# Performance work log

Hardware: AMD Instinct MI355X
Metric: run time of the kernel (lower is better)

## Reference

```python
import jax, jax.numpy as jnp
import numpy as np

N_SKU, N_WH, N_SUP = 100000, 5000, 2000
D_IN, D_OUT, H = 128, 64, 4
DH = D_OUT // H  # 16
E_INTRA, E_CROSS = 400000, 200000
EPS_LN = 1e-5


def setup_inputs() -> dict:
    key = jax.random.key(0)
    ks = jax.random.split(key, 40)
    f32 = jnp.float32

    def edges(k, E, n_src, n_dst):
        k1, k2 = jax.random.split(k)
        return jnp.stack([
            jax.random.randint(k1, (E,), 0, n_src),
            jax.random.randint(k2, (E,), 0, n_dst),
        ]).astype(jnp.int32)

    inp = {
        'x_sku': jax.random.normal(ks[0], (N_SKU, D_IN), f32),
        'x_wh': jax.random.normal(ks[1], (N_WH, D_IN), f32),
        'x_sup': jax.random.normal(ks[2], (N_SUP, D_IN), f32),
    }
    names = ['plant', 'pg', 'sg', 'st', 'ship', 'supply']
    for i, nm in enumerate(names):
        inp['W_' + nm] = jax.random.normal(ks[3 + 2 * i], (D_IN, D_OUT), f32) * 0.05
        inp['a_' + nm] = jax.random.normal(ks[4 + 2 * i], (2 * DH,), f32) * 0.05
    inp['proj_W'] = jax.random.normal(ks[20], (2 * D_OUT, D_OUT), f32) * 0.05
    inp['proj_b'] = jnp.zeros((D_OUT,), f32)
    inp['ln_g'] = jnp.ones((D_OUT,), f32)
    inp['ln_b'] = jnp.zeros((D_OUT,), f32)
    inp['res_W'] = jax.random.normal(ks[21], (D_IN, D_OUT), f32) * 0.05
    inp['ei_plant'] = edges(ks[22], E_INTRA, N_SKU, N_SKU)
    inp['ei_pg'] = edges(ks[23], E_INTRA, N_SKU, N_SKU)
    inp['ei_sg'] = edges(ks[24], E_INTRA, N_SKU, N_SKU)
    inp['ei_st'] = edges(ks[25], E_INTRA, N_SKU, N_SKU)
    inp['ei_ship'] = edges(ks[26], E_CROSS, N_SKU, N_WH)
    inp['ei_supply'] = edges(ks[27], E_CROSS, N_SKU, N_SUP)
    return inp


def _gat_conv(src_feat, dst_feat, ei, W, a, num_dst):
    """One-edge-type multi-head GAT: ELU edge scores, per-dst softmax, scatter-add."""
    src_i, dst_i = ei[0], ei[1]
    h_src = (src_feat @ W).reshape(-1, H, DH)  # [N_src, H, dh]
    h_dst = (dst_feat @ W).reshape(-1, H, DH)  # [N_dst, H, dh]
    hs = h_src[src_i]  # [E, H, dh] gather
    hd = h_dst[dst_i]  # [E, H, dh]
    # a^T [h_src || h_dst], shared attention vector across heads
    e = jax.nn.elu(hs @ a[:DH] + hd @ a[DH:])  # [E, H]
    # numerically stable scatter-softmax over edges grouped by dst node
    e_max = jax.lax.stop_gradient(jax.ops.segment_max(e, dst_i, num_segments=num_dst))
    e_max = jnp.where(jnp.isfinite(e_max), e_max, 0.0)
    exp_e = jnp.exp(e - e_max[dst_i])
    denom = jax.ops.segment_sum(exp_e, dst_i, num_segments=num_dst)
    alpha = exp_e / (denom[dst_i] + 1e-12)  # [E, H]
    out = jax.ops.segment_sum(alpha[..., None] * hs, dst_i, num_segments=num_dst)
    return out.reshape(num_dst, D_OUT)


def reference(x_sku, x_wh, x_sup,
              W_plant, a_plant, W_pg, a_pg, W_sg, a_sg, W_st, a_st,
              W_ship, a_ship, W_supply, a_supply,
              proj_W, proj_b, ln_g, ln_b, res_W,
              ei_plant, ei_pg, ei_sg, ei_st, ei_ship, ei_supply):
    # branch A (intra sku->sku edge types), summed into sku accumulator
    oa_sku = (_gat_conv(x_sku, x_sku, ei_plant, W_plant, a_plant, N_SKU)
              + _gat_conv(x_sku, x_sku, ei_pg, W_pg, a_pg, N_SKU)
              + _gat_conv(x_sku, x_sku, ei_sg, W_sg, a_sg, N_SKU)
              + _gat_conv(x_sku, x_sku, ei_st, W_st, a_st, N_SKU))
    ob_sku = jnp.zeros((N_SKU, D_OUT), x_sku.dtype)
    # branch B (cross edge types)
    oa_wh = jnp.zeros((N_WH, D_OUT), x_wh.dtype)
    ob_wh = _gat_conv(x_sku, x_wh, ei_ship, W_ship, a_ship, N_WH)
    oa_sup = jnp.zeros((N_SUP, D_OUT), x_sup.dtype)
    ob_sup = _gat_conv(x_sku, x_sup, ei_supply, W_supply, a_supply, N_SUP)

    def finish(x, oa, ob):
        y = jnp.concatenate([oa, ob], axis=-1) @ proj_W + proj_b + x @ res_W
        mu = y.mean(-1, keepdims=True)
        var = ((y - mu) ** 2).mean(-1, keepdims=True)
        return (y - mu) / jnp.sqrt(var + EPS_LN) * ln_g + ln_b

    return (finish(x_sku, oa_sku, ob_sku),
            finish(x_wh, oa_wh, ob_wh),
            finish(x_sup, oa_sup, ob_sup))
```

## Files before the change

### kernel.cpp

```cpp
#include <hip/hip_runtime.h>
#include <hip/hip_bf16.h>
#include <cstdint>

#define NS 100000
#define NW 5000
#define NPS 2000
#define DI 128
#define DO 64
#define NSTRIPS (NS/16)
#define NFLAT (4*NS + NW + NPS)
#define NWPAD 5008
#define NBUK 134
#define BCAP 20480
#define CHUNK 8192

#define B_CONV 6688
#define B_PACK 304
#define B_SWH  157
#define B_SSUP 63

typedef unsigned short bfu;
typedef __attribute__((ext_vector_type(8))) short s8v;
typedef __attribute__((ext_vector_type(4))) float f4v;

__device__ inline bfu f2bf(float f) {
  uint32_t u = __float_as_uint(f);
  u = (u + 0x7FFFu + ((u >> 16) & 1u)) >> 16;
  return (bfu)u;
}
__device__ inline float bf2f(bfu u) {
  return __uint_as_float((uint32_t)u << 16);
}

struct ESeg { const int* ei[6]; int E[6]; int Ecum[7]; };

__device__ inline void buk_of(int t, int d, int& b, int& loc) {
  if (t < 4)       { int f = d * 4 + t; b = f >> 12;        loc = f & 4095; }
  else if (t == 4) { b = 98 + (d >> 8);                     loc = d & 255; }
  else             { b = 118 + (d >> 7);                    loc = d & 127; }
}

struct PackA {
  const float* W[6]; const float* a[6];
  const float* resW; const float* projW;
  bfu* Bp; bfu* Rp; bfu* Pp;
};

struct K1Args {
  ESeg S; int* gCur; uint32_t* binned; int ETOT; int nbin;
  const float* x0; bfu* o0; int n0;
  const float* x1; bfu* o1; int n1;
  const float* x2; bfu* o2; int n2;
  PackA P;
  const float* xwh; const float* xsup; float* sd_wh; float* sd_sup;
};

__device__ void bin_body(const K1Args& A, int bid) {
  __shared__ int cnt[NBUK];
  __shared__ int runb[NBUK];
  const ESeg& S = A.S;
  int tid = threadIdx.x;
  int gbase = bid * CHUNK;
  if (tid < NBUK) cnt[tid] = 0;
  __syncthreads();
  #pragma unroll 4
  for (int i = 0; i < CHUNK / 256; ++i) {
    int g = gbase + i * 256 + tid;
    if (g < A.ETOT) {
      int t = 0;
      #pragma unroll
      for (int k = 0; k < 5; ++k) t += (g >= S.Ecum[k + 1]);
      int e = g - S.Ecum[t];
      int d = S.ei[t][S.E[t] + e];
      int b, loc; buk_of(t, d, b, loc);
      atomicAdd(&cnt[b], 1);
    }
  }
  __syncthreads();
  if (tid < NBUK) { runb[tid] = atomicAdd(&A.gCur[tid], cnt[tid]); cnt[tid] = 0; }
  __syncthreads();
  #pragma unroll 4
  for (int i = 0; i < CHUNK / 256; ++i) {
    int g = gbase + i * 256 + tid;
    if (g < A.ETOT) {
      int t = 0;
      #pragma unroll
      for (int k = 0; k < 5; ++k) t += (g >= S.Ecum[k + 1]);
      int e = g - S.Ecum[t];
      int sv = S.ei[t][e];
      int d  = S.ei[t][S.E[t] + e];
      int b, loc; buk_of(t, d, b, loc);
      int pos = runb[b] + atomicAdd(&cnt[b], 1);
      if (pos < BCAP)
        A.binned[(size_t)b * BCAP + pos] = ((uint32_t)loc << 17) | (uint32_t)sv;
    }
  }
}

__device__ void convert_body(const K1Args& A, int bid) {
  int t = bid * 256 + threadIdx.x;
  const float* x; bfu* o; int i;
  if (t < A.n0) { x = A.x0; o = A.o0; i = t; }
  else if (t < A.n0 + A.n1) { x = A.x1; o = A.o1; i = t - A.n0; }
  else if (t < A.n0 + A.n1 + A.n2) { x = A.x2; o = A.o2; i = t - A.n0 - A.n1; }
  else return;
  const float4* p = (const float4*)x + (size_t)i * 2;
  float4 a = p[0], b = p[1];
  uint4 v;
  v.x = (uint32_t)f2bf(a.x) | ((uint32_t)f2bf(a.y) << 16);
  v.y = (uint32_t)f2bf(a.z) | ((uint32_t)f2bf(a.w) << 16);
  v.z = (uint32_t)f2bf(b.x) | ((uint32_t)f2bf(b.y) << 16);
  v.w = (uint32_t)f2bf(b.z) | ((uint32_t)f2bf(b.w) << 16);
  ((uint4*)o)[i] = v;
}

__device__ void pack_body(const PackA& P, int bid) {
  int t = bid * 256 + threadIdx.x;
  if (t < 61440) {
    int ty = t / 10240, rem = t % 10240;
    int r = rem / 128, k = rem % 128;
    const float* W = P.W[ty]; const float* a = P.a[ty];
    float v = 0.f;
    if (r < 64) v = W[k * 64 + r];
    else if (r < 72) {
      int h = (r - 64) & 3;
      const float* av = (r < 68) ? a : (a + 16);
      #pragma unroll
      for (int m = 0; m < 16; ++m) v += W[k * 64 + h * 16 + m] * av[m];
    }
    P.Bp[ty * 10240 + rem] = f2bf(v);
  } else if (t < 69632) {
    int i = t - 61440; int j = i / 128, k = i % 128;
    P.Rp[i] = f2bf(P.resW[k * 64 + j]);
  } else if (t < 77824) {
    int i = t - 69632; int j = i / 128, k = i % 128;
    P.Pp[i] = f2bf(P.projW[k * 64 + j]);
  }
}

__device__ void scores_body(const float* __restrict__ x, const float* __restrict__ W,
                            const float* __restrict__ a, float* __restrict__ sdst,
                            int N, int bid, int nblk) {
  int tid = threadIdx.x;
  int lane = tid & 63;
  float wa[4] = {0.f, 0.f, 0.f, 0.f}, wb[4] = {0.f, 0.f, 0.f, 0.f};
  for (int m = 0; m < 16; ++m) {
    float av = a[16 + m];
    #pragma unroll
    for (int h = 0; h < 4; ++h) {
      wa[h] += W[lane * 64 + h * 16 + m] * av;
      wb[h] += W[(64 + lane) * 64 + h * 16 + m] * av;
    }
  }
  int w  = (bid * 256 + tid) >> 6;
  int nw = (nblk * 256) >> 6;
  for (int n = w; n < N; n += nw) {
    float xa = x[(size_t)n * 128 + lane], xc = x[(size_t)n * 128 + 64 + lane];
    float4 r;
    r.x = xa * wa[0] + xc * wb[0]; r.y = xa * wa[1] + xc * wb[1];
    r.z = xa * wa[2] + xc * wb[2]; r.w = xa * wa[3] + xc * wb[3];
    #pragma unroll
    for (int m = 1; m < 64; m <<= 1) {
      r.x += __shfl_xor(r.x, m); r.y += __shfl_xor(r.y, m);
      r.z += __shfl_xor(r.z, m); r.w += __shfl_xor(r.w, m);
    }
    if (lane == 0) ((float4*)sdst)[n] = r;
  }
}

__global__ __launch_bounds__(256) void k_front(K1Args A) {
  int bid = blockIdx.x;
  if (bid < A.nbin) { bin_body(A, bid); return; }
  bid -= A.nbin;
  if (bid < B_CONV) { convert_body(A, bid); return; }
  bid -= B_CONV;
  if (bid < B_PACK) { pack_body(A.P, bid); return; }
  bid -= B_PACK;
  if (bid < B_SWH) { scores_body(A.xwh, A.P.W[4], A.P.a[4], A.sd_wh, NW, bid, B_SWH); return; }
  bid -= B_SWH;
  scores_body(A.xsup, A.P.W[5], A.P.a[5], A.sd_sup, NPS, bid, B_SSUP);
}

struct MidArgs {
  const int* gCur; const uint32_t* binned; int* offs; int* ssorted;
  const bfu* xb; const bfu* Bp;
  bfu* hbAll; float* ssAll; float* sdAll; int nstrips;
};

__device__ void csr_body(const MidArgs& M, int b) {
  __shared__ int hist[4096];
  __shared__ int wq[4];
  __shared__ int wsc[4];
  __shared__ int bbase_s, cnt_s;
  int tid = threadIdx.x;
  int lane = tid & 63, wid = tid >> 6;
  int cthis = (tid < NBUK) ? min(M.gCur[tid], BCAP) : 0;
  int incx = cthis;
  #pragma unroll
  for (int d = 1; d < 64; d <<= 1) { int t = __shfl_up(incx, d); if (lane >= d) incx += t; }
  if (lane == 63) wq[wid] = incx;
  #pragma unroll
  for (int k = 0; k < 16; ++k) hist[tid * 16 + k] = 0;
  __syncthreads();
  int wp = 0;
  for (int k = 0; k < wid; ++k) wp += wq[k];
  if (tid == b) { int inclusive = incx + wp; bbase_s = inclusive - cthis; cnt_s = cthis; }
  __syncthreads();
  int cnt = cnt_s, bbase = bbase_s;
  const uint32_t* bk = M.binned + (size_t)b * BCAP;
  for (int i = tid; i < cnt; i += 256)
    atomicAdd(&hist[bk[i] >> 17], 1);
  __syncthreads();
  int t16 = tid * 16;
  int v[16], tsum = 0;
  #pragma unroll
  for (int k = 0; k < 16; ++k) { v[k] = hist[t16 + k]; tsum += v[k]; }
  int inc = tsum;
  #pragma unroll
  for (int d = 1; d < 64; d <<= 1) { int t = __shfl_up(inc, d); if (lane >= d) inc += t; }
  if (lane == 63) wsc[wid] = inc;
  __syncthreads();
  int wpre = 0;
  for (int k = 0; k < wid; ++k) wpre += wsc[k];
  int run = inc - tsum + wpre;
  #pragma unroll
  for (int k = 0; k < 16; ++k) { hist[t16 + k] = run; run += v[k]; }
  __syncthreads();
  int sbase, nslots;
  if (b < 98)        { sbase = b << 12;                nslots = min(4096, 4 * NS - sbase); }
  else if (b < 118)  { int lb = (b - 98) << 8;  sbase = 4 * NS + lb;      nslots = min(256, NW - lb); }
  else               { int lb = (b - 118) << 7; sbase = 4 * NS + NW + lb; nslots = min(128, NPS - lb); }
  for (int i = tid; i < nslots; i += 256) M.offs[sbase + i] = bbase + hist[i];
  if (b == NBUK - 1 && tid == 0) M.offs[NFLAT] = bbase + cnt;
  __syncthreads();
  for (int i = tid; i < cnt; i += 256) {
    uint32_t vv = bk[i];
    int p = atomicAdd(&hist[vv >> 17], 1);
    M.ssorted[bbase + p] = (int)(vv & 0x1FFFFu);
  }
}

__device__ void gemm_body(const MidArgs& G, int bloc) {
  int p = bloc >> 9;
  int bsub = bloc & 511;
  const bfu* Bp0 = G.Bp + (size_t)(2 * p) * 10240;
  const bfu* Bp1 = G.Bp + (size_t)(2 * p + 1) * 10240;
  bfu* hb0 = G.hbAll + (size_t)(2 * p) * NS * 64;
  bfu* hb1 = G.hbAll + (size_t)(2 * p + 1) * NS * 64;
  float* ss0 = G.ssAll + (size_t)(2 * p) * NS * 4;
  float* ss1 = G.ssAll + (size_t)(2 * p + 1) * NS * 4;
  float* sd0 = G.sdAll + (size_t)(2 * p) * NS * 4;
  float* sd1 = G.sdAll + (size_t)(2 * p + 1) * NS * 4;
  int lane = threadIdx.x & 63;
  int l15 = lane & 15, q = lane >> 4;
  int w  = (int)((bsub * 256 + threadIdx.x) >> 6);
  int nw = (512 * 256) >> 6;
  s8v bfr[10][4];
  #pragma unroll
  for (int nt = 0; nt < 5; ++nt)
    #pragma unroll
    for (int kq = 0; kq < 4; ++kq) {
      bfr[nt][kq]     = *(const s8v*)(Bp0 + (size_t)(nt * 16 + l15) * 128 + kq * 32 + q * 8);
      bfr[5 + nt][kq] = *(const s8v*)(Bp1 + (size_t)(nt * 16 + l15) * 128 + kq * 32 + q * 8);
    }
  for (int s = w; s < G.nstrips; s += nw) {
    int mb = s * 16;
    f4v acc[10];
    #pragma unroll
    for (int u = 0; u < 10; ++u) acc[u] = (f4v){0.f, 0.f, 0.f, 0.f};
    const bfu* ar = G.xb + (size_t)(mb + l15) * 128 + q * 8;
    #pragma unroll
    for (int kq = 0; kq < 4; ++kq) {
      s8v af = *(const s8v*)(ar + kq * 32);
      #pragma unroll
      for (int u = 0; u < 10; ++u)
        acc[u] = __builtin_amdgcn_mfma_f32_16x16x32_bf16(af, bfr[u][kq], acc[u], 0, 0, 0);
    }
    #pragma unroll
    for (int u = 0; u < 10; ++u) {
      int nt = (u < 5) ? u : u - 5;
      bfu* hb = (u < 5) ? hb0 : hb1;
      float* ssrc = (u < 5) ? ss0 : ss1;
      float* sdst = (u < 5) ? sd0 : sd1;
      int c = nt * 16 + l15;
      #pragma unroll
      for (int r = 0; r < 4; ++r) {
        int node = mb + q * 4 + r;
        float v = acc[u][r];
        if (c < 64)      hb[(size_t)node * 64 + c] = f2bf(v);
        else if (c < 68) ssrc[(size_t)node * 4 + (c - 64)] = v;
        else if (c < 72) sdst[(size_t)node * 4 + (c - 68)] = v;
      }
    }
  }
}

__global__ __launch_bounds__(256, 2) void k_mid(MidArgs M) {
  int bid = blockIdx.x;
  if (bid < NBUK) { csr_body(M, bid); return; }
  gemm_body(M, bid - NBUK);
}

struct AggArgs {
  const int* offs; const int* srcs;
  const bfu* hbAll;
  const float* ssAll;
  const float* sdAll;
  const float* sd_wh; const float* sd_sup;
  bfu* osku; bfu* owh; bfu* osup;
};

__global__ __launch_bounds__(256) void k_megaagg(AggArgs A) {
  int lane = threadIdx.x & 63;
  int q = lane >> 4, m = lane & 15, h = m >> 2;
  int hh = m & 3;
  int i0 = m >> 2;
  int qsh = q << 4;
  int sl0 = qsh + h;
  int w  = (int)((blockIdx.x * 256 + threadIdx.x) >> 6);
  int nw = (int)((gridDim.x * 256) >> 6);
  for (int n = w; n < NS + NW + NPS; n += nw) {
    if (n < NS) {
      const int* ob = A.offs + (size_t)n * 4;
      int4 o = *(const int4*)ob;
      int o4 = ob[4];
      int sb = (q == 0) ? o.x : (q == 1) ? o.y : (q == 2) ? o.z : o.w;
      int se = (q == 0) ? o.y : (q == 1) ? o.z : (q == 2) ? o.w : o4;
      int len = se - sb;
      int maxlen = max(max(o.y - o.x, o.z - o.y), max(o.w - o.z, o4 - o.w));
      float sdq = A.sdAll[((size_t)q * NS + n) * 4 + hh];
      uint32_t tbase = (uint32_t)q * (uint32_t)NS;
      float den = 0.f, a0 = 0.f, a1 = 0.f, a2 = 0.f, a3 = 0.f;
      for (int j0 = 0; j0 < maxlen; j0 += 16) {
        int ei = j0 + m;
        int sidx = (ei < len) ? A.srcs[sb + ei] : 0;
        int gmax = min(16, maxlen - j0);
        for (int jj = 0; jj < gmax; jj += 8) {
          int sA = __shfl(sidx, qsh + jj + i0);
          int sB = __shfl(sidx, qsh + jj + 4 + i0);
          float scA = A.ssAll[(tbase + (uint32_t)sA) * 4u + (uint32_t)hh];
          float scB = A.ssAll[(tbase + (uint32_t)sB) * 4u + (uint32_t)hh];
          float eA = scA + sdq, eB = scB + sdq;
          eA = eA > 0.f ? eA : (__expf(eA) - 1.f);
          eB = eB > 0.f ? eB : (__expf(eB) - 1.f);
          float wA = (j0 + jj + i0)     < len ? __expf(eA) : 0.f;
          float wB = (j0 + jj + 4 + i0) < len ? __expf(eB) : 0.f;
          uint2 hv[8]; float wg[8];
          #pragma unroll
          for (int i = 0; i < 8; ++i) {
            int s = __shfl(sidx, qsh + jj + i);
            uint32_t nb = tbase + (uint32_t)s;
            hv[i] = *(const uint2*)(A.hbAll + nb * 64u + (uint32_t)(m * 4));
            wg[i] = __shfl((i & 4) ? wB : wA, sl0 + ((i & 3) << 2));
          }
          #pragma unroll
          for (int i = 0; i < 8; ++i) {
            float wgt = wg[i];
            den += wgt;
            a0 = fmaf(__uint_as_float(hv[i].x << 16), wgt, a0);
            a1 = fmaf(__uint_as_float(hv[i].x & 0xffff0000u), wgt, a1);
            a2 = fmaf(__uint_as_float(hv[i].y << 16), wgt, a2);
            a3 = fmaf(__uint_as_float(hv[i].y & 0xffff0000u), wgt, a3);
          }
        }
      }
      float inv = __builtin_amdgcn_rcpf(den + 1e-12f);
      float r0 = a0 * inv, r1 = a1 * inv, r2 = a2 * inv, r3 = a3 * inv;
      r0 += __shfl_xor(r0, 16); r0 += __shfl_xor(r0, 32);
      r1 += __shfl_xor(r1, 16); r1 += __shfl_xor(r1, 32);
      r2 += __shfl_xor(r2, 16); r2 += __shfl_xor(r2, 32);
      r3 += __shfl_xor(r3, 16); r3 += __shfl_xor(r3, 32);
      if (q == 0) {
        uint2 pk;
        pk.x = (uint32_t)f2bf(r0) | ((uint32_t)f2bf(r1) << 16);
        pk.y = (uint32_t)f2bf(r2) | ((uint32_t)f2bf(r3) << 16);
        *(uint2*)(A.osku + (size_t)n * 64 + m * 4) = pk;
      }
    } else {
      int tt, nl; const float* sd; bfu* op;
      int fi;
      if (n < NS + NW) { tt = 4; nl = n - NS; fi = 4 * NS + nl; sd = A.sd_wh; op = A.owh + (size_t)nl * 64; }
      else { tt = 5; nl = n - NS - NW; fi = 4 * NS + NW + nl; sd = A.sd_sup; op = A.osup + (size_t)nl * 64; }
      int beg = A.offs[fi], end = A.offs[fi + 1];
      uint32_t tbase = (uint32_t)tt * (uint32_t)NS;
      float sdq = sd[(size_t)nl * 4 + hh];
      float den = 0.f, a0 = 0.f, a1 = 0.f, a2 = 0.f, a3 = 0.f;
      for (int cb = beg; cb < end; cb += 64) {
        int rem = min(64, end - cb);
        int sidx = (lane < rem) ? A.srcs[cb + lane] : 0;
        for (int jb = 0; jb < rem; jb += 32) {
          int eA = jb + 4 * i0 + q;
          int sA = __shfl(sidx, eA);
          int sB = __shfl(sidx, eA + 16);
          float scA = A.ssAll[(tbase + (uint32_t)sA) * 4u + (uint32_t)hh];
          float scB = A.ssAll[(tbase + (uint32_t)sB) * 4u + (uint32_t)hh];
          float fA = scA + sdq, fB = scB + sdq;
          fA = fA > 0.f ? fA : (__expf(fA) - 1.f);
          fB = fB > 0.f ? fB : (__expf(fB) - 1.f);
          float wA = (eA)      < rem ? __expf(fA) : 0.f;
          float wB = (eA + 16) < rem ? __expf(fB) : 0.f;
          uint2 hv[8]; float wg[8];
          #pragma unroll
          for (int i = 0; i < 8; ++i) {
            int s = __shfl(sidx, jb + 4 * i + q);
            uint32_t nb = tbase + (uint32_t)s;
            hv[i] = *(const uint2*)(A.hbAll + nb * 64u + (uint32_t)(m * 4));
            wg[i] = __shfl((i & 4) ? wB : wA, sl0 + ((i & 3) << 2));
          }
          #pragma unroll
          for (int i = 0; i < 8; ++i) {
            float wgt = wg[i];
            den += wgt;
            a0 = fmaf(__uint_as_float(hv[i].x << 16), wgt, a0);
            a1 = fmaf(__uint_as_float(hv[i].x & 0xffff0000u), wgt, a1);
            a2 = fmaf(__uint_as_float(hv[i].y << 16), wgt, a2);
            a3 = fmaf(__uint_as_float(hv[i].y & 0xffff0000u), wgt, a3);
          }
        }
      }
      den += __shfl_xor(den, 16); den += __shfl_xor(den, 32);
      a0 += __shfl_xor(a0, 16); a0 += __shfl_xor(a0, 32);
      a1 += __shfl_xor(a1, 16); a1 += __shfl_xor(a1, 32);
      a2 += __shfl_xor(a2, 16); a2 += __shfl_xor(a2, 32);
      a3 += __shfl_xor(a3, 16); a3 += __shfl_xor(a3, 32);
      float inv = __builtin_amdgcn_rcpf(den + 1e-12f);
      if (q == 0) {
        uint2 pk;
        pk.x = (uint32_t)f2bf(a0 * inv) | ((uint32_t)f2bf(a1 * inv) << 16);
        pk.y = (uint32_t)f2bf(a2 * inv) | ((uint32_t)f2bf(a3 * inv) << 16);
        *(uint2*)(op + m * 4) = pk;
      }
    }
  }
}

struct FinArgs {
  const bfu* agg0; const bfu* agg1; const bfu* agg2;
  const bfu* x0; const bfu* x1; const bfu* x2;
  float* out0; float* out1; float* out2;
  const bfu* Pp; const bfu* Rp;
  const float* pb; const float* g; const float* bb;
  int bcut0, bcut1;
};

__global__ __launch_bounds__(256) void k_finish(FinArgs F) {
  int bid = blockIdx.x;
  int role = (bid >= F.bcut0) + (bid >= F.bcut1);
  int b0 = (role == 0) ? 0 : (role == 1) ? F.bcut0 : F.bcut1;
  int nb = (role == 0) ? F.bcut0 : (role == 1) ? (F.bcut1 - F.bcut0) : ((int)gridDim.x - F.bcut1);
  int bloc = bid - b0;
  const bfu* aggb = (role == 0) ? F.agg0 : (role == 1) ? F.agg1 : F.agg2;
  const bfu* xbf  = (role == 0) ? F.x0 : (role == 1) ? F.x1 : F.x2;
  float* outp     = (role == 0) ? F.out0 : (role == 1) ? F.out1 : F.out2;
  int koff    = (role == 0) ? 0 : 64;
  int N       = (role == 0) ? NS : (role == 1) ? NW : NPS;
  int nstrips = (role == 0) ? NSTRIPS : (role == 1) ? (NWPAD / 16) : (NPS / 16);

  int lane = threadIdx.x & 63, l15 = lane & 15, q = lane >> 4;
  int w  = (int)((bloc * 256 + threadIdx.x) >> 6);
  int nw = nb << 2;
  s8v bP[4][2], bR[4][4];
  float pbv[4], gv[4], bv[4];
  #pragma unroll
  for (int c = 0; c < 4; ++c) {
    const bfu* pr = F.Pp + (size_t)(c * 16 + l15) * 128 + koff;
    bP[c][0] = *(const s8v*)(pr + q * 8);
    bP[c][1] = *(const s8v*)(pr + 32 + q * 8);
    const bfu* rr = F.Rp + (size_t)(c * 16 + l15) * 128;
    #pragma unroll
    for (int kq = 0; kq < 4; ++kq) bR[c][kq] = *(const s8v*)(rr + kq * 32 + q * 8);
    pbv[c] = F.pb[c * 16 + l15]; gv[c] = F.g[c * 16 + l15]; bv[c] = F.bb[c * 16 + l15];
  }
  for (int s = w; s < nstrips; s += nw) {
    int mb = s * 16;
    const bfu* ar = aggb + (size_t)(mb + l15) * 64 + q * 8;
    const bfu* xr = xbf + (size_t)(mb + l15) * 128 + q * 8;
    s8v a0 = *(const s8v*)ar, a1 = *(const s8v*)(ar + 32);
    s8v x0 = *(const s8v*)xr, x1 = *(const s8v*)(xr + 32),
        x2 = *(const s8v*)(xr + 64), x3 = *(const s8v*)(xr + 96);
    f4v acc[4];
    #pragma unroll
    for (int c = 0; c < 4; ++c) {
      acc[c] = (f4v){0.f, 0.f, 0.f, 0.f};
      acc[c] = __builtin_amdgcn_mfma_f32_16x16x32_bf16(a0, bP[c][0], acc[c], 0, 0, 0);
      acc[c] = __builtin_amdgcn_mfma_f32_16x16x32_bf16(a1, bP[c][1], acc[c], 0, 0, 0);
      acc[c] = __builtin_amdgcn_mfma_f32_16x16x32_bf16(x0, bR[c][0], acc[c], 0, 0, 0);
      acc[c] = __builtin_amdgcn_mfma_f32_16x16x32_bf16(x1, bR[c][1], acc[c], 0, 0, 0);
      acc[c] = __builtin_amdgcn_mfma_f32_16x16x32_bf16(x2, bR[c][2], acc[c], 0, 0, 0);
      acc[c] = __builtin_amdgcn_mfma_f32_16x16x32_bf16(x3, bR[c][3], acc[c], 0, 0, 0);
    }
    #pragma unroll
    for (int r = 0; r < 4; ++r) {
      int row = mb + q * 4 + r;
      float y0 = acc[0][r] + pbv[0], y1 = acc[1][r] + pbv[1];
      float y2 = acc[2][r] + pbv[2], y3 = acc[3][r] + pbv[3];
      float s1 = y0 + y1 + y2 + y3;
      s1 += __shfl_xor(s1, 1); s1 += __shfl_xor(s1, 2);
      s1 += __shfl_xor(s1, 4); s1 += __shfl_xor(s1, 8);
      float mu = s1 * 0.015625f;
      float d0 = y0 - mu, d1 = y1 - mu, d2 = y2 - mu, d3 = y3 - mu;
      float s2 = d0 * d0 + d1 * d1 + d2 * d2 + d3 * d3;
      s2 += __shfl_xor(s2, 1); s2 += __shfl_xor(s2, 2);
      s2 += __shfl_xor(s2, 4); s2 += __shfl_xor(s2, 8);
      float rs = rsqrtf(s2 * 0.015625f + 1e-5f);
      if (row < N) {
        float* orow = outp + (size_t)row * 64 + l15;
        orow[0]  = d0 * rs * gv[0] + bv[0];
        orow[16] = d1 * rs * gv[1] + bv[1];
        orow[32] = d2 * rs * gv[2] + bv[2];
        orow[48] = d3 * rs * gv[3] + bv[3];
      }
    }
  }
}

extern "C" void kernel_launch(void* const* d_in, const int* in_sizes, int n_in,
                              void* d_out, int out_size, void* d_ws, size_t ws_size,
                              hipStream_t stream) {
  const float* x_sku = (const float*)d_in[0];
  const float* x_wh  = (const float*)d_in[1];
  const float* x_sup = (const float*)d_in[2];
  const float* Wt[6]; const float* at[6];
  for (int t = 0; t < 6; ++t) { Wt[t] = (const float*)d_in[3 + 2 * t]; at[t] = (const float*)d_in[4 + 2 * t]; }
  const float* projW = (const float*)d_in[15];
  const float* projb = (const float*)d_in[16];
  const float* lng   = (const float*)d_in[17];
  const float* lnb   = (const float*)d_in[18];
  const float* resW  = (const float*)d_in[19];
  const int* ei[6]; int Et[6];
  for (int t = 0; t < 6; ++t) { ei[t] = (const int*)d_in[20 + t]; Et[t] = in_sizes[20 + t] / 2; }
  float* out = (float*)d_out;

  int ETOT = 0;
  for (int t = 0; t < 6; ++t) ETOT += Et[t];

  char* ws = (char*)d_ws;
  size_t off = 0;
  auto alloc = [&](size_t bytes) { off = (off + 255) & ~(size_t)255; void* p = ws + off; off += bytes; return p; };

  bfu*  xb      = (bfu*)alloc((size_t)NS * DI * 2);
  bfu*  xb_wh   = (bfu*)alloc((size_t)NWPAD * DI * 2);
  bfu*  xb_sup  = (bfu*)alloc((size_t)NPS * DI * 2);
  bfu*  Bp      = (bfu*)alloc((size_t)6 * 80 * 128 * 2);
  bfu*  Rp      = (bfu*)alloc((size_t)64 * 128 * 2);
  bfu*  Pp      = (bfu*)alloc((size_t)64 * 128 * 2);
  bfu*  hbAll   = (bfu*)alloc((size_t)6 * NS * 64 * 2);
  float* ssAll  = (float*)alloc((size_t)6 * NS * 4 * 4);
  float* sdAll  = (float*)alloc((size_t)6 * NS * 4 * 4);
  float* sdst_wh  = (float*)alloc((size_t)NW * 4 * 4);
  float* sdst_sup = (float*)alloc((size_t)NPS * 4 * 4);
  size_t agg_bytes = ((size_t)NS + NWPAD + NPS) * 64 * 2;
  size_t bin_bytes = (size_t)NBUK * BCAP * 4;
  char* un = (char*)alloc(agg_bytes > bin_bytes ? agg_bytes : bin_bytes);
  bfu* agg_sku = (bfu*)un;
  bfu* agg_wh  = agg_sku + (size_t)NS * 64;
  bfu* agg_sup = agg_wh + (size_t)NWPAD * 64;
  uint32_t* binned = (uint32_t*)un;
  int* gCur    = (int*)alloc(256 * 4);
  int* offsb   = (int*)alloc((size_t)(NFLAT + 1) * 4);
  int* ssorted = (int*)alloc((size_t)ETOT * 4);

  hipMemsetAsync(gCur, 0, NBUK * 4, stream);

  K1Args K;
  K.S.Ecum[0] = 0;
  for (int t = 0; t < 6; ++t) { K.S.ei[t] = ei[t]; K.S.E[t] = Et[t]; K.S.Ecum[t + 1] = K.S.Ecum[t] + Et[t]; }
  K.gCur = gCur; K.binned = binned; K.ETOT = ETOT;
  K.nbin = (ETOT + CHUNK - 1) / CHUNK;
  K.x0 = x_sku; K.o0 = xb;     K.n0 = NS * 16;
  K.x1 = x_wh;  K.o1 = xb_wh;  K.n1 = NW * 16;
  K.x2 = x_sup; K.o2 = xb_sup; K.n2 = NPS * 16;
  for (int t = 0; t < 6; ++t) { K.P.W[t] = Wt[t]; K.P.a[t] = at[t]; }
  K.P.resW = resW; K.P.projW = projW; K.P.Bp = Bp; K.P.Rp = Rp; K.P.Pp = Pp;
  K.xwh = x_wh; K.xsup = x_sup; K.sd_wh = sdst_wh; K.sd_sup = sdst_sup;
  int gfront = K.nbin + B_CONV + B_PACK + B_SWH + B_SSUP;
  k_front<<<gfront, 256, 0, stream>>>(K);

  MidArgs M;
  M.gCur = gCur; M.binned = binned; M.offs = offsb; M.ssorted = ssorted;
  M.xb = xb; M.Bp = Bp; M.hbAll = hbAll; M.ssAll = ssAll; M.sdAll = sdAll; M.nstrips = NSTRIPS;
  k_mid<<<NBUK + 1536, 256, 0, stream>>>(M);

  AggArgs A;
  A.offs = offsb; A.srcs = ssorted;
  A.hbAll = hbAll; A.ssAll = ssAll; A.sdAll = sdAll;
  A.sd_wh = sdst_wh; A.sd_sup = sdst_sup;
  A.osku = agg_sku; A.owh = agg_wh; A.osup = agg_sup;
  k_megaagg<<<(NS + NW + NPS + 3) / 4, 256, 0, stream>>>(A);

  FinArgs F;
  F.agg0 = agg_sku; F.agg1 = agg_wh; F.agg2 = agg_sup;
  F.x0 = xb; F.x1 = xb_wh; F.x2 = xb_sup;
  F.out0 = out; F.out1 = out + (size_t)NS * 64; F.out2 = out + (size_t)(NS + NW) * 64;
  F.Pp = Pp; F.Rp = Rp; F.pb = projb; F.g = lng; F.bb = lnb;
  F.bcut0 = 1563; F.bcut1 = 1563 + 79;
  k_finish<<<1563 + 79 + 32, 256, 0, stream>>>(F);
}
```

Before: 382.3 us.

## Stage binned edges in LDS for coalesced bucket writes; cap aggregation grid

The edge-binning pass now counting-sorts each chunk by bucket in shared memory, using a wave-level prefix scan. It then writes every bucket's run to global memory contiguously, replacing the old scattered per-edge global stores. The chunk size is halved so the staging arrays fit in LDS, which doubles the number of binning blocks and the global atomics on bucket cursors. Separately, the aggregation kernel launches a fixed 2048 blocks instead of one block per four nodes. That is only correct if the kernel strides over the remaining nodes.

After: 378.0 us. No clear change (-1.1%).

```diff
diff --git a/kernel.cpp b/kernel.cpp
--- a/kernel.cpp
+++ b/kernel.cpp
@@ -12,7 +12,7 @@
 #define NWPAD 5008
 #define NBUK 134
 #define BCAP 20480
-#define CHUNK 8192
+#define CHUNK 4096
 
 #define B_CONV 6688
 #define B_PACK 304
@@ -56,16 +56,22 @@
 };
 
 __device__ void bin_body(const K1Args& A, int bid) {
+  __shared__ uint32_t stage[CHUNK];
+  __shared__ unsigned char bstage[CHUNK];
   __shared__ int cnt[NBUK];
-  __shared__ int runb[NBUK];
+  __shared__ int lstart[NBUK];
+  __shared__ int cur[NBUK];
+  __shared__ int gbase[NBUK];
+  __shared__ int wq[4];
   const ESeg& S = A.S;
   int tid = threadIdx.x;
-  int gbase = bid * CHUNK;
+  int lane = tid & 63, wid = tid >> 6;
+  int ebase = bid * CHUNK;
   if (tid < NBUK) cnt[tid] = 0;
   __syncthreads();
-  #pragma unroll 4
+  #pragma unroll
   for (int i = 0; i < CHUNK / 256; ++i) {
-    int g = gbase + i * 256 + tid;
+    int g = ebase + i * 256 + tid;
     if (g < A.ETOT) {
       int t = 0;
       #pragma unroll
@@ -77,11 +83,24 @@
     }
   }
   __syncthreads();
-  if (tid < NBUK) { runb[tid] = atomicAdd(&A.gCur[tid], cnt[tid]); cnt[tid] = 0; }
-  __syncthreads();
-  #pragma unroll 4
+  int c = (tid < NBUK) ? cnt[tid] : 0;
+  int inc = c;
+  #pragma unroll
+  for (int d = 1; d < 64; d <<= 1) { int t = __shfl_up(inc, d); if (lane >= d) inc += t; }
+  if (lane == 63) wq[wid] = inc;
+  __syncthreads();
+  int wp = 0;
+  for (int k = 0; k < wid; ++k) wp += wq[k];
+  int excl = inc - c + wp;
+  if (tid < NBUK) {
+    lstart[tid] = excl;
+    cur[tid] = excl;
+    gbase[tid] = atomicAdd(&A.gCur[tid], c);
+  }
+  __syncthreads();
+  #pragma unroll
   for (int i = 0; i < CHUNK / 256; ++i) {
-    int g = gbase + i * 256 + tid;
+    int g = ebase + i * 256 + tid;
     if (g < A.ETOT) {
       int t = 0;
       #pragma unroll
@@ -90,10 +109,18 @@
       int sv = S.ei[t][e];
       int d  = S.ei[t][S.E[t] + e];
       int b, loc; buk_of(t, d, b, loc);
-      int pos = runb[b] + atomicAdd(&cnt[b], 1);
-      if (pos < BCAP)
-        A.binned[(size_t)b * BCAP + pos] = ((uint32_t)loc << 17) | (uint32_t)sv;
-    }
+      int p = atomicAdd(&cur[b], 1);
+      stage[p] = ((uint32_t)loc << 17) | (uint32_t)sv;
+      bstage[p] = (unsigned char)b;
+    }
+  }
+  __syncthreads();
+  int tot = min(CHUNK, A.ETOT - ebase);
+  for (int i = tid; i < tot; i += 256) {
+    int b = bstage[i];
+    int pos = gbase[b] + (i - lstart[b]);
+    if (pos < BCAP)
+      A.binned[(size_t)b * BCAP + pos] = stage[i];
   }
 }
 
@@ -586,7 +613,7 @@
   A.hbAll = hbAll; A.ssAll = ssAll; A.sdAll = sdAll;
   A.sd_wh = sdst_wh; A.sd_sup = sdst_sup;
   A.osku = agg_sku; A.owh = agg_wh; A.osup = agg_sup;
-  k_megaagg<<<(NS + NW + NPS + 3) / 4, 256, 0, stream>>>(A);
+  k_megaagg<<<2048, 256, 0, stream>>>(A);
 
   FinArgs F;
   F.agg0 = agg_sku; F.agg1 = agg_wh; F.agg2 = agg_sup;
```
